# Kernel optimization log

Measured on AMD Instinct MI355X. Metric: run time of the kernel, lower is better.

Reference implementation:

```python
import jax, jax.numpy as jnp
import numpy as np

B, T, C = 2, 2048, 1024
H = 16
HS = C // H  # head_size = 64


def setup_inputs() -> dict:
    key = jax.random.key(0)
    k1, k2, k3 = jax.random.split(key, 3)
    x = jax.random.normal(k1, (B, T, C), dtype=jnp.float32)
    # nn.Linear(n_embd, 3*n_embd): weight [3C, C], bias [3C]
    W = jax.random.normal(k2, (3 * C, C), dtype=jnp.float32) * (C ** -0.5)
    b = jax.random.normal(k3, (3 * C,), dtype=jnp.float32) * 0.02
    return {"x": x, "W": W, "b": b}


def reference(x, W, b):
    Bs, Ts, Cs = x.shape
    # fused QKV projection: [B,T,3C]
    qkv = x @ W.T + b
    qkv = qkv.reshape(Bs, Ts, 3, H, HS)
    q, k, v = jnp.moveaxis(qkv, 2, 0)          # each [B,T,H,HS]
    q = q.transpose(0, 2, 1, 3)                 # [B,H,T,HS]
    k = k.transpose(0, 2, 1, 3)
    v = v.transpose(0, 2, 1, 3)
    scale = HS ** -0.5
    wei = jnp.einsum('bhqd,bhkd->bhqk', q, k) * scale  # [B,H,T,T]
    causal = jnp.tril(jnp.ones((Ts, Ts), dtype=bool))
    wei = jnp.where(causal, wei, -jnp.inf)
    wei = jax.nn.softmax(wei, axis=-1)
    out = jnp.einsum('bhqk,bhkd->bhqd', wei, v)        # [B,H,T,HS]
    return out.transpose(0, 2, 1, 3).reshape(Bs, Ts, Cs)
```

## Files before the change

kernel.cpp:

```cpp
#include <hip/hip_runtime.h>
#include <hip/hip_bf16.h>

typedef __attribute__((ext_vector_type(8))) short bf16x8;
typedef __attribute__((ext_vector_type(4))) float f32x4;

#define BATCH 2
#define T_SEQ 2048
#define C_EMB 1024
#define NH 16
#define HS 64

__device__ __forceinline__ void gld_lds16(const __hip_bfloat16* g, void* l) {
    __builtin_amdgcn_global_load_lds((const __attribute__((address_space(1))) uint32_t*)g,
                                     (__attribute__((address_space(3))) uint32_t*)l, 16, 0, 0);
}

__global__ void cvt_f32_bf16(const float4* __restrict__ s0, ushort4* __restrict__ d0, int n40,
                             const float4* __restrict__ s1, ushort4* __restrict__ d1, int n41) {
    int i = blockIdx.x * blockDim.x + threadIdx.x;
    const float4* s; ushort4* d; int j;
    if (i < n40)            { s = s0; d = d0; j = i; }
    else if (i < n40 + n41) { s = s1; d = d1; j = i - n40; }
    else return;
    float4 v = s[j];
    ushort4 o;
    __hip_bfloat16 h;
    h = __float2bfloat16(v.x); o.x = *(ushort*)&h;
    h = __float2bfloat16(v.y); o.y = *(ushort*)&h;
    h = __float2bfloat16(v.z); o.z = *(ushort*)&h;
    h = __float2bfloat16(v.w); o.w = *(ushort*)&h;
    d[j] = o;
}

#define NT_K 16

__launch_bounds__(512, 2)
__global__ void qkv_gemm(const __hip_bfloat16* __restrict__ xb,
                         const __hip_bfloat16* __restrict__ wb,
                         const float* __restrict__ bias,
                         __hip_bfloat16* __restrict__ qo,
                         __hip_bfloat16* __restrict__ ko,
                         __hip_bfloat16* __restrict__ vto)
{
    __shared__ __align__(16) char smem[131072];
    __hip_bfloat16* ASB = (__hip_bfloat16*)smem;
    __hip_bfloat16* BSB = (__hip_bfloat16*)(smem + 65536);
    const int K = C_EMB;
    const int nTn = (3 * C_EMB) / 256;
    int bid = blockIdx.x;
    int wgid = (bid & 7) * 24 + (bid >> 3);
    int bm = wgid / nTn, bn = wgid % nTn;
    int m0 = bm * 256, n0 = bn * 256;
    int tid  = threadIdx.x;
    int lane = tid & 63, w = tid >> 6;
    int wr = w >> 2, wc = w & 3;
    int c = lane & 15, g = lane >> 4;
    int sr = lane >> 2;
    int sj = (lane & 3) ^ ((sr >> 1) & 3);
    int rchnk = (g ^ ((c >> 1) & 3)) << 4;

#define STAGE_A(kt, kh, buf) \
    { _Pragma("unroll") for (int i_ = 0; i_ < 2; ++i_) { \
        int r0_ = w * 32 + i_ * 16; \
        gld_lds16(&xb[(size_t)(m0 + r0_ + sr) * K + (kt) * 64 + (kh) * 32 + sj * 8], \
                  &ASB[((buf) * 2 + (kh)) * 8192 + r0_ * 32]); } }
#define STAGE_B(kt, kh, buf) \
    { _Pragma("unroll") for (int i_ = 0; i_ < 2; ++i_) { \
        int r0_ = w * 32 + i_ * 16; \
        gld_lds16(&wb[(size_t)(n0 + r0_ + sr) * K + (kt) * 64 + (kh) * 32 + sj * 8], \
                  &BSB[((buf) * 2 + (kh)) * 8192 + r0_ * 32]); } }

    f32x4 acc[8][4];
#pragma unroll
    for (int mi = 0; mi < 8; ++mi)
#pragma unroll
        for (int ni = 0; ni < 4; ++ni)
            acc[mi][ni] = (f32x4){0.f, 0.f, 0.f, 0.f};

    STAGE_A(0, 0, 0); STAGE_B(0, 0, 0);
    STAGE_A(0, 1, 0); STAGE_B(0, 1, 0);
    STAGE_A(1, 0, 1); STAGE_B(1, 0, 1);
    asm volatile("s_waitcnt vmcnt(4)" ::: "memory");
    __builtin_amdgcn_s_barrier();

    for (int t = 0; t < NT_K; ++t) {
        int buf = t & 1;
#pragma unroll
        for (int ks = 0; ks < 2; ++ks) {
            const __hip_bfloat16* AL = &ASB[(buf * 2 + ks) * 8192];
            const __hip_bfloat16* BL = &BSB[(buf * 2 + ks) * 8192];
            bf16x8 af[8], bfr[4];
#pragma unroll
            for (int mi = 0; mi < 8; ++mi)
                af[mi] = *(const bf16x8*)((const char*)AL + (wr * 128 + mi * 16 + c) * 64 + rchnk);
#pragma unroll
            for (int ni = 0; ni < 4; ++ni)
                bfr[ni] = *(const bf16x8*)((const char*)BL + (wc * 64 + ni * 16 + c) * 64 + rchnk);
            if (ks == 0) {
                if (t + 1 < NT_K) { STAGE_A(t + 1, 1, buf ^ 1); STAGE_B(t + 1, 1, buf ^ 1); }
            } else {
                if (t + 2 < NT_K) { STAGE_A(t + 2, 0, buf); STAGE_B(t + 2, 0, buf); }
            }
            __builtin_amdgcn_s_barrier();
            asm volatile("s_waitcnt lgkmcnt(0)" ::: "memory");
            __builtin_amdgcn_s_setprio(1);
#pragma unroll
            for (int mi = 0; mi < 8; ++mi)
#pragma unroll
                for (int ni = 0; ni < 4; ++ni)
                    acc[mi][ni] = __builtin_amdgcn_mfma_f32_16x16x32_bf16(af[mi], bfr[ni], acc[mi][ni], 0, 0, 0);
            __builtin_amdgcn_s_setprio(0);
            if (ks == 1) {
                if (t + 2 < NT_K) asm volatile("s_waitcnt vmcnt(4)" ::: "memory");
                else              asm volatile("s_waitcnt vmcnt(0)" ::: "memory");
            }
            __builtin_amdgcn_s_barrier();
        }
    }
#undef STAGE_A
#undef STAGE_B

    const float QSCALE = 0.125f * 1.44269504088896340736f;
    if (bn < 8) {
        const bool isQ = (bn < 4);
        __hip_bfloat16* dst = isQ ? qo : ko;
        float scale = isQ ? QSCALE : 1.0f;
        int h = (bn * 4 + wc) & (NH - 1);
        int b = m0 >> 11;
        size_t bhb = (size_t)(b * NH + h) * T_SEQ;
#pragma unroll
        for (int ni = 0; ni < 4; ++ni) {
            int d = ni * 16 + c;
            float bv = bias[n0 + wc * 64 + d];
#pragma unroll
            for (int mi = 0; mi < 8; ++mi) {
#pragma unroll
                for (int r = 0; r < 4; ++r) {
                    int tt = (m0 & (T_SEQ - 1)) + wr * 128 + mi * 16 + g * 4 + r;
                    float v = (acc[mi][ni][r] + bv) * scale;
                    dst[(bhb + tt) * HS + d] = __float2bfloat16(v);
                }
            }
        }
    } else {
        __syncthreads();
        char* tb = smem + w * 16384;
        int h = (bn - 8) * 4 + wc;
#pragma unroll
        for (int ni = 0; ni < 4; ++ni) {
            int d = ni * 16 + c;
            float bv = bias[n0 + wc * 64 + d];
#pragma unroll
            for (int mi = 0; mi < 8; ++mi) {
#pragma unroll
                for (int r = 0; r < 4; ++r) {
                    int m = mi * 16 + g * 4 + r;
                    __hip_bfloat16 hv = __float2bfloat16(acc[mi][ni][r] + bv);
                    *(ushort*)(tb + d * 256 + (((m >> 3) ^ c) << 4) + (m & 7) * 2) = *(ushort*)&hv;
                }
            }
        }
        int b = m0 >> 11;
        int t0 = (m0 & (T_SEQ - 1)) + wr * 128;
        size_t bh = (size_t)(b * NH + h);
        int c2 = lane & 15, g2 = lane >> 4;
#pragma unroll
        for (int it = 0; it < 16; ++it) {
            int d = it * 4 + g2;
            bf16x8 vv = *(bf16x8*)(tb + d * 256 + ((c2 ^ (d & 15)) << 4));
            *(bf16x8*)(&vto[(bh * HS + d) * T_SEQ + t0 + c2 * 8]) = vv;
        }
    }
}

__launch_bounds__(256, 4)
__global__ void attn_fwd(const __hip_bfloat16* __restrict__ qb,
                         const __hip_bfloat16* __restrict__ kb,
                         const __hip_bfloat16* __restrict__ vtb,
                         float* __restrict__ out)
{
    __shared__ __align__(16) char smem[40960];

    int idx = blockIdx.x;
    int bh = idx & 31;
    int qt = 31 - (idx >> 5);
    int w  = threadIdx.x >> 6;
    int lane = threadIdx.x & 63;
    int c = lane & 15, g = lane >> 4;
    char* p_strip = smem + 32768 + w * 2048;

    const __hip_bfloat16* Qp = qb  + (size_t)bh * T_SEQ * HS;
    const __hip_bfloat16* Kp = kb  + (size_t)bh * T_SEQ * HS;
    const __hip_bfloat16* Vp = vtb + (size_t)bh * HS * T_SEQ;
    int b = bh >> 4, h = bh & (NH - 1);

    int srow = lane >> 3;
    int scol = ((lane & 7) ^ srow) << 3;
    int swz  = (c & 7) << 4;
    int krow0 = w * 16 + srow;
    int krow1 = w * 16 + 8 + srow;
    int qw = qt * 64 + w * 16;
    int ntile = qt + 1;

    bf16x8 qf[2];
    qf[0] = *(const bf16x8*)(&Qp[(size_t)(qw + c) * HS + g * 8]);
    qf[1] = *(const bf16x8*)(&Qp[(size_t)(qw + c) * HS + 32 + g * 8]);

    f32x4 oacc[4];
#pragma unroll
    for (int i = 0; i < 4; ++i) oacc[i] = (f32x4){0.f, 0.f, 0.f, 0.f};
    float lrow = 0.f;

#define ATT_STAGE(t_, buf_) { \
    int k0_ = (t_) * 64; \
    char* kb_ = smem + (buf_) * 8192; \
    char* vb_ = smem + 16384 + (buf_) * 8192; \
    gld_lds16(&Kp[(size_t)(k0_ + krow0) * HS + scol],  kb_ + (w * 16) * 128); \
    gld_lds16(&Kp[(size_t)(k0_ + krow1) * HS + scol],  kb_ + (w * 16 + 8) * 128); \
    gld_lds16(&Vp[(size_t)krow0 * T_SEQ + k0_ + scol], vb_ + (w * 16) * 128); \
    gld_lds16(&Vp[(size_t)krow1 * T_SEQ + k0_ + scol], vb_ + (w * 16 + 8) * 128); }

    ATT_STAGE(0, 0);

    for (int tix = 0; tix < ntile; ++tix) {
        int cur = tix & 1;
        asm volatile("s_waitcnt vmcnt(0)" ::: "memory");
        __builtin_amdgcn_s_barrier();
        if (tix + 1 < ntile) ATT_STAGE(tix + 1, cur ^ 1);

        bool diag = (tix == ntile - 1);
        const char* KL = smem + cur * 8192;
        const char* VL = smem + 16384 + cur * 8192;

        f32x4 sacc[4];
#pragma unroll
        for (int i = 0; i < 4; ++i) sacc[i] = (f32x4){0.f, 0.f, 0.f, 0.f};
        __builtin_amdgcn_s_setprio(1);
#pragma unroll
        for (int ks = 0; ks < 2; ++ks)
#pragma unroll
            for (int kc = 0; kc < 4; ++kc)
                if (!diag || kc <= w) {
                    int rr = kc * 16 + c;
                    int colB = (ks * 64 + g * 16) ^ swz;
                    bf16x8 kf = *(const bf16x8*)(KL + rr * 128 + colB);
                    sacc[kc] = __builtin_amdgcn_mfma_f32_16x16x32_bf16(kf, qf[ks], sacc[kc], 0, 0, 0);
                }
        __builtin_amdgcn_s_setprio(0);

#pragma unroll
        for (int kc = 0; kc < 4; ++kc) {
            float p0, p1, p2, p3;
            if (!diag) {
                p0 = __builtin_amdgcn_exp2f(sacc[kc][0]);
                p1 = __builtin_amdgcn_exp2f(sacc[kc][1]);
                p2 = __builtin_amdgcn_exp2f(sacc[kc][2]);
                p3 = __builtin_amdgcn_exp2f(sacc[kc][3]);
            } else {
                int kbase = kc * 16 + g * 4;
                int lim = w * 16 + c;
                p0 = (kc <= w && kbase + 0 <= lim) ? __builtin_amdgcn_exp2f(sacc[kc][0]) : 0.f;
                p1 = (kc <= w && kbase + 1 <= lim) ? __builtin_amdgcn_exp2f(sacc[kc][1]) : 0.f;
                p2 = (kc <= w && kbase + 2 <= lim) ? __builtin_amdgcn_exp2f(sacc[kc][2]) : 0.f;
                p3 = (kc <= w && kbase + 3 <= lim) ? __builtin_amdgcn_exp2f(sacc[kc][3]) : 0.f;
            }
            lrow += (p0 + p1) + (p2 + p3);
            unsigned lo = ((__builtin_bit_cast(unsigned, p0) + 0x8000u) >> 16) |
                          ((__builtin_bit_cast(unsigned, p1) + 0x8000u) & 0xffff0000u);
            unsigned hi = ((__builtin_bit_cast(unsigned, p2) + 0x8000u) >> 16) |
                          ((__builtin_bit_cast(unsigned, p3) + 0x8000u) & 0xffff0000u);
            int gran = ((kc * 2 + (g >> 1)) ^ (c & 7)) << 4;
            *(uint2*)(p_strip + c * 128 + gran + ((g & 1) << 3)) = make_uint2(lo, hi);
        }

        int ksm = diag ? ((w >= 2) ? 2 : 1) : 2;
        __builtin_amdgcn_s_setprio(1);
#pragma unroll
        for (int ks = 0; ks < 2; ++ks) {
            if (ks >= ksm) break;
            int pgran = ((ks * 4 + g) ^ (c & 7)) << 4;
            bf16x8 pf = *(bf16x8*)(p_strip + c * 128 + pgran);
#pragma unroll
            for (int d16 = 0; d16 < 4; ++d16) {
                int dr = d16 * 16 + c;
                int colB = (ks * 64 + g * 16) ^ swz;
                bf16x8 vf = *(const bf16x8*)(VL + dr * 128 + colB);
                oacc[d16] = __builtin_amdgcn_mfma_f32_16x16x32_bf16(vf, pf, oacc[d16], 0, 0, 0);
            }
        }
        __builtin_amdgcn_s_setprio(0);
    }

    float v = lrow;
    v += __shfl_xor(v, 16, 64);
    v += __shfl_xor(v, 32, 64);
    float linv = 1.0f / v;
    float* orow = &out[((size_t)(b * T_SEQ + qw + c)) * C_EMB + h * HS + g * 4];
#pragma unroll
    for (int d16 = 0; d16 < 4; ++d16) {
        float4 st;
        st.x = oacc[d16][0] * linv;
        st.y = oacc[d16][1] * linv;
        st.z = oacc[d16][2] * linv;
        st.w = oacc[d16][3] * linv;
        *(float4*)(&orow[d16 * 16]) = st;
    }
#undef ATT_STAGE
}

extern "C" void kernel_launch(void* const* d_in, const int* in_sizes, int n_in,
                              void* d_out, int out_size, void* d_ws, size_t ws_size,
                              hipStream_t stream) {
    const float* x    = (const float*)d_in[0];
    const float* W    = (const float*)d_in[1];
    const float* bias = (const float*)d_in[2];
    float* out = (float*)d_out;

    char* ws = (char*)d_ws;
    __hip_bfloat16* xb  = (__hip_bfloat16*)(ws);
    __hip_bfloat16* wb  = (__hip_bfloat16*)(ws + (8u  << 20));
    __hip_bfloat16* qo  = (__hip_bfloat16*)(ws + (14u << 20));
    __hip_bfloat16* ko  = (__hip_bfloat16*)(ws + (22u << 20));
    __hip_bfloat16* vto = (__hip_bfloat16*)(ws + (30u << 20));

    int n4x = BATCH * T_SEQ * C_EMB / 4;
    int n4w = 3 * C_EMB * C_EMB / 4;
    int n4  = n4x + n4w;
    cvt_f32_bf16<<<(n4 + 255) / 256, 256, 0, stream>>>(
        (const float4*)x, (ushort4*)xb, n4x,
        (const float4*)W, (ushort4*)wb, n4w);

    int gemm_grid = (BATCH * T_SEQ / 256) * (3 * C_EMB / 256);
    qkv_gemm<<<gemm_grid, 512, 0, stream>>>(xb, wb, bias, qo, ko, vto);

    attn_fwd<<<1024, 256, 0, stream>>>(qo, ko, vto, out);
}
```

Before: 78.99 us.

## Split long causal query tiles across two blocks and add a reduce kernel

The 16 longest query tiles per head are each split into two halves of the key range, run as separate blocks, which raises the attention grid from 1024 to 1536 blocks and shortens the longest block. The first half writes an unnormalized partial output and its row sums to workspace. The second half writes its unnormalized output straight into the output buffer with its own row sums. A new reduce kernel adds the two partials and normalizes. This targets load imbalance from the causal triangle, and pays for it with extra global traffic (about 8 MB of partials plus a read-modify-write of the output) and one more kernel launch. It also reuses workspace regions that earlier stages have finished with.

```diff
diff --git a/kernel.cpp b/kernel.cpp
--- a/kernel.cpp
+++ b/kernel.cpp
@@ -177,13 +177,26 @@
 __global__ void attn_fwd(const __hip_bfloat16* __restrict__ qb,
                          const __hip_bfloat16* __restrict__ kb,
                          const __hip_bfloat16* __restrict__ vtb,
-                         float* __restrict__ out)
+                         float* __restrict__ out,
+                         float* __restrict__ ws_part,
+                         float* __restrict__ ws_l0,
+                         float* __restrict__ ws_l1)
 {
     __shared__ __align__(16) char smem[40960];
 
     int idx = blockIdx.x;
     int bh = idx & 31;
-    int qt = 31 - (idx >> 5);
+    int j  = idx >> 5;
+    int qt, c0, c1, mode;
+    if (j < 32) {
+        qt = 31 - (j >> 1);
+        int hsp = (qt + 2) >> 1;
+        if ((j & 1) == 0) { c0 = 0; c1 = hsp; mode = 1; }
+        else             { c0 = hsp; c1 = qt + 1; mode = 2; }
+    } else {
+        qt = 47 - j;
+        c0 = 0; c1 = qt + 1; mode = 0;
+    }
     int w  = threadIdx.x >> 6;
     int lane = threadIdx.x & 63;
     int c = lane & 15, g = lane >> 4;
@@ -200,7 +213,6 @@
     int krow0 = w * 16 + srow;
     int krow1 = w * 16 + 8 + srow;
     int qw = qt * 64 + w * 16;
-    int ntile = qt + 1;
 
     bf16x8 qf[2];
     qf[0] = *(const bf16x8*)(&Qp[(size_t)(qw + c) * HS + g * 8]);
@@ -220,15 +232,15 @@
     gld_lds16(&Vp[(size_t)krow0 * T_SEQ + k0_ + scol], vb_ + (w * 16) * 128); \
     gld_lds16(&Vp[(size_t)krow1 * T_SEQ + k0_ + scol], vb_ + (w * 16 + 8) * 128); }
 
-    ATT_STAGE(0, 0);
-
-    for (int tix = 0; tix < ntile; ++tix) {
-        int cur = tix & 1;
+    ATT_STAGE(c0, 0);
+
+    for (int tix = c0; tix < c1; ++tix) {
+        int cur = (tix - c0) & 1;
         asm volatile("s_waitcnt vmcnt(0)" ::: "memory");
         __builtin_amdgcn_s_barrier();
-        if (tix + 1 < ntile) ATT_STAGE(tix + 1, cur ^ 1);
-
-        bool diag = (tix == ntile - 1);
+        if (tix + 1 < c1) ATT_STAGE(tix + 1, cur ^ 1);
+
+        bool diag = (tix == qt);
         const char* KL = smem + cur * 8192;
         const char* VL = smem + 16384 + cur * 8192;
 
@@ -294,18 +306,64 @@
     float v = lrow;
     v += __shfl_xor(v, 16, 64);
     v += __shfl_xor(v, 32, 64);
-    float linv = 1.0f / v;
-    float* orow = &out[((size_t)(b * T_SEQ + qw + c)) * C_EMB + h * HS + g * 4];
-#pragma unroll
-    for (int d16 = 0; d16 < 4; ++d16) {
-        float4 st;
-        st.x = oacc[d16][0] * linv;
-        st.y = oacc[d16][1] * linv;
-        st.z = oacc[d16][2] * linv;
-        st.w = oacc[d16][3] * linv;
-        *(float4*)(&orow[d16 * 16]) = st;
+
+    int lr = w * 16 + c;
+    if (mode == 0) {
+        float linv = 1.0f / v;
+        float* orow = &out[((size_t)(b * T_SEQ + qw + c)) * C_EMB + h * HS + g * 4];
+#pragma unroll
+        for (int d16 = 0; d16 < 4; ++d16) {
+            float4 st;
+            st.x = oacc[d16][0] * linv;
+            st.y = oacc[d16][1] * linv;
+            st.z = oacc[d16][2] * linv;
+            st.w = oacc[d16][3] * linv;
+            *(float4*)(&orow[d16 * 16]) = st;
+        }
+    } else {
+        int pid = (qt - 16) * 32 + bh;
+        if (mode == 1) {
+            float* pO = ws_part + (size_t)pid * 4096;
+#pragma unroll
+            for (int d16 = 0; d16 < 4; ++d16) {
+                float4 st;
+                st.x = oacc[d16][0]; st.y = oacc[d16][1];
+                st.z = oacc[d16][2]; st.w = oacc[d16][3];
+                *(float4*)(&pO[lr * 64 + d16 * 16 + g * 4]) = st;
+            }
+            if (g == 0) ws_l0[pid * 64 + lr] = v;
+        } else {
+            float* orow = &out[((size_t)(b * T_SEQ + qw + c)) * C_EMB + h * HS + g * 4];
+#pragma unroll
+            for (int d16 = 0; d16 < 4; ++d16) {
+                float4 st;
+                st.x = oacc[d16][0]; st.y = oacc[d16][1];
+                st.z = oacc[d16][2]; st.w = oacc[d16][3];
+                *(float4*)(&orow[d16 * 16]) = st;
+            }
+            if (g == 0) ws_l1[pid * 64 + lr] = v;
+        }
     }
 #undef ATT_STAGE
+}
+
+__global__ void attn_reduce(float* __restrict__ out, const float* __restrict__ part,
+                            const float* __restrict__ l0, const float* __restrict__ l1) {
+    int idx = blockIdx.x * 256 + threadIdx.x;
+    int pid = idx >> 10;
+    int rem = idx & 1023;
+    int lr = rem >> 4, f4 = (rem & 15) * 4;
+    int qt = 16 + (pid >> 5), bh = pid & 31;
+    int b = bh >> 4, h = bh & (NH - 1);
+    float linv = 1.0f / (l0[pid * 64 + lr] + l1[pid * 64 + lr]);
+    float* dst = &out[((size_t)(b * T_SEQ + qt * 64 + lr)) * C_EMB + h * HS + f4];
+    float4 a = *(float4*)dst;
+    float4 p = *(const float4*)(&part[(size_t)pid * 4096 + lr * 64 + f4]);
+    a.x = (a.x + p.x) * linv;
+    a.y = (a.y + p.y) * linv;
+    a.z = (a.z + p.z) * linv;
+    a.w = (a.w + p.w) * linv;
+    *(float4*)dst = a;
 }
 
 extern "C" void kernel_launch(void* const* d_in, const int* in_sizes, int n_in,
@@ -322,6 +380,9 @@
     __hip_bfloat16* qo  = (__hip_bfloat16*)(ws + (14u << 20));
     __hip_bfloat16* ko  = (__hip_bfloat16*)(ws + (22u << 20));
     __hip_bfloat16* vto = (__hip_bfloat16*)(ws + (30u << 20));
+    float* ws_part = (float*)(ws);
+    float* ws_l0   = (float*)(ws + (8u << 20));
+    float* ws_l1   = (float*)(ws + (8u << 20) + (1u << 17));
 
     int n4x = BATCH * T_SEQ * C_EMB / 4;
     int n4w = 3 * C_EMB * C_EMB / 4;
@@ -333,5 +394,6 @@
     int gemm_grid = (BATCH * T_SEQ / 256) * (3 * C_EMB / 256);
     qkv_gemm<<<gemm_grid, 512, 0, stream>>>(xb, wb, bias, qo, ko, vto);
 
-    attn_fwd<<<1024, 256, 0, stream>>>(qo, ko, vto, out);
-}
+    attn_fwd<<<1536, 256, 0, stream>>>(qo, ko, vto, out, ws_part, ws_l0, ws_l1);
+    attn_reduce<<<2048, 256, 0, stream>>>(out, ws_part, ws_l0, ws_l1);
+}
```

Measured after the change: 90.59 us. +14.7%, slower.

## Shrink QKV GEMM N-tile to 192 so the grid fills 256 CUs

Applied to the files above, without the earlier changes.

Changes the QKV projection GEMM tile from 256x256 to 256x192, raising the grid from 192 to 256 workgroups to match the MI355X CU count and avoid a partial wave. B staging, LDS sizing, per-wave wait counts and the Q/K/V epilogue are reworked because a tile now spans heads and sections at 16-column granularity. The V transpose now goes through per-fragment LDS scratch. This costs less reuse per tile and uneven load work across waves.

```diff
diff --git a/kernel.cpp b/kernel.cpp
--- a/kernel.cpp
+++ b/kernel.cpp
@@ -42,15 +42,15 @@
                          __hip_bfloat16* __restrict__ ko,
                          __hip_bfloat16* __restrict__ vto)
 {
-    __shared__ __align__(16) char smem[131072];
+    __shared__ __align__(16) char smem[114688];
     __hip_bfloat16* ASB = (__hip_bfloat16*)smem;
     __hip_bfloat16* BSB = (__hip_bfloat16*)(smem + 65536);
     const int K = C_EMB;
-    const int nTn = (3 * C_EMB) / 256;
+    const int nTn = (3 * C_EMB) / 192;
     int bid = blockIdx.x;
-    int wgid = (bid & 7) * 24 + (bid >> 3);
+    int wgid = (bid & 7) * 32 + (bid >> 3);
     int bm = wgid / nTn, bn = wgid % nTn;
-    int m0 = bm * 256, n0 = bn * 256;
+    int m0 = bm * 256, n0 = bn * 192;
     int tid  = threadIdx.x;
     int lane = tid & 63, w = tid >> 6;
     int wr = w >> 2, wc = w & 3;
@@ -65,22 +65,28 @@
         gld_lds16(&xb[(size_t)(m0 + r0_ + sr) * K + (kt) * 64 + (kh) * 32 + sj * 8], \
                   &ASB[((buf) * 2 + (kh)) * 8192 + r0_ * 32]); } }
 #define STAGE_B(kt, kh, buf) \
-    { _Pragma("unroll") for (int i_ = 0; i_ < 2; ++i_) { \
-        int r0_ = w * 32 + i_ * 16; \
-        gld_lds16(&wb[(size_t)(n0 + r0_ + sr) * K + (kt) * 64 + (kh) * 32 + sj * 8], \
-                  &BSB[((buf) * 2 + (kh)) * 8192 + r0_ * 32]); } }
-
-    f32x4 acc[8][4];
+    { if (w < 4) { \
+        gld_lds16(&wb[(size_t)(n0 + w * 32 + sr) * K + (kt) * 64 + (kh) * 32 + sj * 8], \
+                  &BSB[((buf) * 2 + (kh)) * 6144 + (w * 32) * 32]); \
+        gld_lds16(&wb[(size_t)(n0 + w * 32 + 16 + sr) * K + (kt) * 64 + (kh) * 32 + sj * 8], \
+                  &BSB[((buf) * 2 + (kh)) * 6144 + (w * 32 + 16) * 32]); \
+      } else { \
+        gld_lds16(&wb[(size_t)(n0 + 128 + (w - 4) * 16 + sr) * K + (kt) * 64 + (kh) * 32 + sj * 8], \
+                  &BSB[((buf) * 2 + (kh)) * 6144 + (128 + (w - 4) * 16) * 32]); \
+      } }
+
+    f32x4 acc[8][3];
 #pragma unroll
     for (int mi = 0; mi < 8; ++mi)
 #pragma unroll
-        for (int ni = 0; ni < 4; ++ni)
+        for (int ni = 0; ni < 3; ++ni)
             acc[mi][ni] = (f32x4){0.f, 0.f, 0.f, 0.f};
 
     STAGE_A(0, 0, 0); STAGE_B(0, 0, 0);
     STAGE_A(0, 1, 0); STAGE_B(0, 1, 0);
     STAGE_A(1, 0, 1); STAGE_B(1, 0, 1);
-    asm volatile("s_waitcnt vmcnt(4)" ::: "memory");
+    if (w < 4) asm volatile("s_waitcnt vmcnt(4)" ::: "memory");
+    else       asm volatile("s_waitcnt vmcnt(3)" ::: "memory");
     __builtin_amdgcn_s_barrier();
 
     for (int t = 0; t < NT_K; ++t) {
@@ -88,14 +94,14 @@
 #pragma unroll
         for (int ks = 0; ks < 2; ++ks) {
             const __hip_bfloat16* AL = &ASB[(buf * 2 + ks) * 8192];
-            const __hip_bfloat16* BL = &BSB[(buf * 2 + ks) * 8192];
-            bf16x8 af[8], bfr[4];
+            const __hip_bfloat16* BL = &BSB[(buf * 2 + ks) * 6144];
+            bf16x8 af[8], bfr[3];
 #pragma unroll
             for (int mi = 0; mi < 8; ++mi)
                 af[mi] = *(const bf16x8*)((const char*)AL + (wr * 128 + mi * 16 + c) * 64 + rchnk);
 #pragma unroll
-            for (int ni = 0; ni < 4; ++ni)
-                bfr[ni] = *(const bf16x8*)((const char*)BL + (wc * 64 + ni * 16 + c) * 64 + rchnk);
+            for (int ni = 0; ni < 3; ++ni)
+                bfr[ni] = *(const bf16x8*)((const char*)BL + (wc * 48 + ni * 16 + c) * 64 + rchnk);
             if (ks == 0) {
                 if (t + 1 < NT_K) { STAGE_A(t + 1, 1, buf ^ 1); STAGE_B(t + 1, 1, buf ^ 1); }
             } else {
@@ -107,12 +113,16 @@
 #pragma unroll
             for (int mi = 0; mi < 8; ++mi)
 #pragma unroll
-                for (int ni = 0; ni < 4; ++ni)
+                for (int ni = 0; ni < 3; ++ni)
                     acc[mi][ni] = __builtin_amdgcn_mfma_f32_16x16x32_bf16(af[mi], bfr[ni], acc[mi][ni], 0, 0, 0);
             __builtin_amdgcn_s_setprio(0);
             if (ks == 1) {
-                if (t + 2 < NT_K) asm volatile("s_waitcnt vmcnt(4)" ::: "memory");
-                else              asm volatile("s_waitcnt vmcnt(0)" ::: "memory");
+                if (t + 2 < NT_K) {
+                    if (w < 4) asm volatile("s_waitcnt vmcnt(4)" ::: "memory");
+                    else       asm volatile("s_waitcnt vmcnt(3)" ::: "memory");
+                } else {
+                    asm volatile("s_waitcnt vmcnt(0)" ::: "memory");
+                }
             }
             __builtin_amdgcn_s_barrier();
         }
@@ -121,54 +131,47 @@
 #undef STAGE_B
 
     const float QSCALE = 0.125f * 1.44269504088896340736f;
-    if (bn < 8) {
-        const bool isQ = (bn < 4);
-        __hip_bfloat16* dst = isQ ? qo : ko;
-        float scale = isQ ? QSCALE : 1.0f;
-        int h = (bn * 4 + wc) & (NH - 1);
-        int b = m0 >> 11;
-        size_t bhb = (size_t)(b * NH + h) * T_SEQ;
-#pragma unroll
-        for (int ni = 0; ni < 4; ++ni) {
-            int d = ni * 16 + c;
-            float bv = bias[n0 + wc * 64 + d];
+    __syncthreads();
+    int b = m0 >> 11;
+    int t0 = (m0 & (T_SEQ - 1)) + wr * 128;
+#pragma unroll
+    for (int ni = 0; ni < 3; ++ni) {
+        int nb = n0 + wc * 48 + ni * 16;
+        int s = nb >> 10;
+        int h = (nb >> 6) & (NH - 1);
+        float bv = bias[nb + c];
+        if (s < 2) {
+            __hip_bfloat16* dst = (s == 0) ? qo : ko;
+            float scale = (s == 0) ? QSCALE : 1.0f;
+            int dd = (nb & 63) + c;
+            size_t bhb = (size_t)(b * NH + h) * T_SEQ;
 #pragma unroll
             for (int mi = 0; mi < 8; ++mi) {
 #pragma unroll
                 for (int r = 0; r < 4; ++r) {
-                    int tt = (m0 & (T_SEQ - 1)) + wr * 128 + mi * 16 + g * 4 + r;
-                    float v = (acc[mi][ni][r] + bv) * scale;
-                    dst[(bhb + tt) * HS + d] = __float2bfloat16(v);
+                    int tt = t0 + mi * 16 + g * 4 + r;
+                    dst[(bhb + tt) * HS + dd] = __float2bfloat16((acc[mi][ni][r] + bv) * scale);
                 }
             }
-        }
-    } else {
-        __syncthreads();
-        char* tb = smem + w * 16384;
-        int h = (bn - 8) * 4 + wc;
-#pragma unroll
-        for (int ni = 0; ni < 4; ++ni) {
-            int d = ni * 16 + c;
-            float bv = bias[n0 + wc * 64 + d];
+        } else {
+            int dbase = nb & 63;
+            char* scr = smem + (w * 3 + ni) * 4096;
 #pragma unroll
             for (int mi = 0; mi < 8; ++mi) {
 #pragma unroll
                 for (int r = 0; r < 4; ++r) {
                     int m = mi * 16 + g * 4 + r;
                     __hip_bfloat16 hv = __float2bfloat16(acc[mi][ni][r] + bv);
-                    *(ushort*)(tb + d * 256 + (((m >> 3) ^ c) << 4) + (m & 7) * 2) = *(ushort*)&hv;
+                    *(ushort*)(scr + c * 256 + ((((m >> 3) ^ c) & 15) << 4) + (m & 7) * 2) = *(ushort*)&hv;
                 }
             }
-        }
-        int b = m0 >> 11;
-        int t0 = (m0 & (T_SEQ - 1)) + wr * 128;
-        size_t bh = (size_t)(b * NH + h);
-        int c2 = lane & 15, g2 = lane >> 4;
-#pragma unroll
-        for (int it = 0; it < 16; ++it) {
-            int d = it * 4 + g2;
-            bf16x8 vv = *(bf16x8*)(tb + d * 256 + ((c2 ^ (d & 15)) << 4));
-            *(bf16x8*)(&vto[(bh * HS + d) * T_SEQ + t0 + c2 * 8]) = vv;
+            size_t bh = (size_t)(b * NH + h);
+#pragma unroll
+            for (int p = 0; p < 4; ++p) {
+                int d = p * 4 + g;
+                bf16x8 vv = *(bf16x8*)(scr + d * 256 + (((c ^ d) & 15) << 4));
+                *(bf16x8*)(&vto[(bh * HS + dbase + d) * T_SEQ + t0 + c * 8]) = vv;
+            }
         }
     }
 }
@@ -330,7 +333,7 @@
         (const float4*)x, (ushort4*)xb, n4x,
         (const float4*)W, (ushort4*)wb, n4w);
 
-    int gemm_grid = (BATCH * T_SEQ / 256) * (3 * C_EMB / 256);
+    int gemm_grid = (BATCH * T_SEQ / 256) * (3 * C_EMB / 192);
     qkv_gemm<<<gemm_grid, 512, 0, stream>>>(xb, wb, bias, qo, ko, vto);
 
     attn_fwd<<<1024, 256, 0, stream>>>(qo, ko, vto, out);
```

After: 78.09 us. About the same (-1.1%).
